# Performance work log

Measured on AMD Instinct MI355X. Metric: run time of the kernel, lower is better.

The kernel has to match this reference:

```python
import jax, jax.numpy as jnp
import numpy as np

B, C, H, W = 16, 256, 64, 64
NH, WS = 8, 8  # num_heads, window_size
HD = C // NH   # head_dim = 32


def setup_inputs() -> dict:
    key = jax.random.key(0)
    k1, k2, k3 = jax.random.split(key, 3)
    x = jax.random.normal(k1, (B, C, H, W), dtype=jnp.float32)
    w_qkv = jax.random.normal(k2, (3 * C, C), dtype=jnp.float32) * 0.02  # 1x1 conv, no bias
    w_proj = jax.random.normal(k3, (C, C), dtype=jnp.float32) * 0.02
    return {"x": x, "w_qkv": w_qkv, "w_proj": w_proj, "shift": 1}


def _window_partition(t, ws):
    # [b,c,h,w] -> [b*(h/ws)*(w/ws), ws*ws, c]
    b, c, h, w = t.shape
    t = t.reshape(b, c, h // ws, ws, w // ws, ws)
    t = t.transpose(0, 2, 4, 3, 5, 1)
    return t.reshape(-1, ws * ws, c)


def _window_reverse(t, b, c, h, w, ws):
    t = t.reshape(b, h // ws, w // ws, ws, ws, c)
    t = t.transpose(0, 5, 1, 3, 2, 4)
    return t.reshape(b, c, h, w)


def reference(x, w_qkv, w_proj, shift):
    b, c, h, w = x.shape
    ws = min(WS, h, w)
    shift_size = ws // 2 if (shift and ws > 1 and h % ws == 0 and w % ws == 0) else 0
    if shift_size > 0:
        x = jnp.roll(x, (-shift_size, -shift_size), axis=(2, 3))
    # 1x1 conv QKV: [b,c,h,w] x [3c,c] -> [b,3c,h,w]
    qkv = jnp.einsum('bchw,oc->bohw', x, w_qkv)
    q, k, v = jnp.split(qkv, 3, axis=1)
    q_t = _window_partition(q, ws)  # [Bw, S, c], S = ws*ws
    k_t = _window_partition(k, ws)
    v_t = _window_partition(v, ws)
    bw, s, _ = q_t.shape
    # heads: [Bw, nh, S, hd]
    qh = q_t.reshape(bw, s, NH, HD).transpose(0, 2, 1, 3)
    kh = k_t.reshape(bw, s, NH, HD).transpose(0, 2, 1, 3)
    vh = v_t.reshape(bw, s, NH, HD).transpose(0, 2, 1, 3)
    scale = 1.0 / jnp.sqrt(jnp.asarray(HD, dtype=qh.dtype))
    scores = jnp.einsum('bnqd,bnkd->bnqk', qh, kh) * scale
    attn = jax.nn.softmax(scores, axis=-1)
    out = jnp.einsum('bnqk,bnkd->bnqd', attn, vh)
    out = out.transpose(0, 2, 1, 3).reshape(bw, s, c)
    out = _window_reverse(out, b, c, h, w, ws)
    if shift_size > 0:
        out = jnp.roll(out, (shift_size, shift_size), axis=(2, 3))
    return jnp.einsum('bchw,oc->bohw', out, w_proj)
```

## Files before the change

### kernel.cpp

```cpp
#include <hip/hip_runtime.h>

typedef short bf16x8 __attribute__((ext_vector_type(8)));
typedef float f32x4 __attribute__((ext_vector_type(4)));
typedef unsigned short u16;
typedef unsigned int u32;

static __device__ __forceinline__ u16 f2bf(float f) {
  u32 u = __builtin_bit_cast(u32, f);
  u32 r = (u + 0x7FFFu + ((u >> 16) & 1u)) >> 16;
  return (u16)r;
}

__global__ __launch_bounds__(256) void k_conv(
    const float* __restrict__ wqkv, const float* __restrict__ wproj,
    u16* __restrict__ wbf) {
  const int cid = blockIdx.x * 256 + threadIdx.x;
  const float* src;
  int dst;
  if (cid < 24576) {
    const int tile = cid >> 9, rem = cid & 511;
    const int k = rem >> 6, lane = rem & 63;
    src = wqkv + (size_t)(tile * 16 + (lane & 15)) * 256 + k * 32 + (lane >> 4) * 8;
    dst = cid;
  } else {
    const int pid = cid - 24576;
    const int mt = pid >> 9, rem = pid & 511;
    const int h = rem >> 6, lane = rem & 63;
    src = wproj + (size_t)(mt * 16 + (lane & 15)) * 256 + h * 32 + (lane >> 4) * 8;
    dst = 24576 + h * 1024 + mt * 64 + lane;
  }
  float4 f0 = *(const float4*)(src);
  float4 f1 = *(const float4*)(src + 4);
  ushort4 a, b;
  a.x = f2bf(f0.x); a.y = f2bf(f0.y); a.z = f2bf(f0.z); a.w = f2bf(f0.w);
  b.x = f2bf(f1.x); b.y = f2bf(f1.y); b.z = f2bf(f1.z); b.w = f2bf(f1.w);
  *(ushort4*)(wbf + (size_t)dst * 8) = a;
  *(ushort4*)(wbf + (size_t)dst * 8 + 4) = b;
}

#define BUF0 0
#define BUF1 4096
#define XB 0
#define QH 8192
#define KH 10752
#define VTH 13312
#define PH 15616
#define LDS_TOT 20224

#define MEMF() asm volatile("" ::: "memory")
#define BAR()                        \
  do {                               \
    MEMF();                          \
    __builtin_amdgcn_s_barrier();    \
    MEMF();                          \
  } while (0)
#define WVM2() asm volatile("s_waitcnt vmcnt(2)" ::: "memory")
#define WVM0() asm volatile("s_waitcnt vmcnt(0)" ::: "memory")
#define WLG0() asm volatile("s_waitcnt lgkmcnt(0)" ::: "memory")

#define GL2LDS(gp, lp)                                   \
  __builtin_amdgcn_global_load_lds(                      \
      (__attribute__((address_space(1))) void*)(gp),     \
      (__attribute__((address_space(3))) void*)(lp), 16, 0, 0)

static __device__ __forceinline__ void stage_half(const u16* g, u16* l, int t) {
#pragma unroll
  for (int j = 0; j < 2; ++j) {
    const int off = (j * 256 + t) * 8;
    GL2LDS(g + off, l + off);
  }
}

#define QKV_TILE(BUFB, DSTB, U)                                           \
  do {                                                                    \
    const u16* wb_ = LDS + (BUFB) + lane * 8;                             \
    f32x4 acc = {0.f, 0.f, 0.f, 0.f};                                     \
    _Pragma("unroll") for (int k = 0; k < 8; ++k) acc =                   \
        __builtin_amdgcn_mfma_f32_16x16x32_bf16(                          \
            af[k], *(const bf16x8*)(wb_ + k * 512), acc, 0, 0, 0);        \
    _Pragma("unroll") for (int r = 0; r < 4; ++r)                         \
        LDS[(DSTB) + (pos0 + r) * 40 + (U) * 16 + l15] = f2bf(acc[r]);    \
  } while (0)

#define V_TILE(BUFB, U)                                                   \
  do {                                                                    \
    const u16* wb_ = LDS + (BUFB) + lane * 8;                             \
    f32x4 acc = {0.f, 0.f, 0.f, 0.f};                                     \
    _Pragma("unroll") for (int k = 0; k < 8; ++k) acc =                   \
        __builtin_amdgcn_mfma_f32_16x16x32_bf16(                          \
            af[k], *(const bf16x8*)(wb_ + k * 512), acc, 0, 0, 0);        \
    ushort4 pk;                                                           \
    pk.x = f2bf(acc[0]); pk.y = f2bf(acc[1]);                             \
    pk.z = f2bf(acc[2]); pk.w = f2bf(acc[3]);                             \
    *(ushort4*)&LDS[VTH + ((U) * 16 + l15) * 72 + pos0] = pk;             \
  } while (0)

__global__ __launch_bounds__(256, 4) void k_fused(
    const float* __restrict__ x, const u16* __restrict__ wbf,
    const int* __restrict__ shiftp, float* __restrict__ out) {
  __shared__ u16 LDS[LDS_TOT];
  const int blk = blockIdx.x;
  const int win = ((blk & 127) << 3) | (blk >> 7);
  const int b = win >> 6, wh = (win >> 3) & 7, ww = win & 7;
  const int off = (shiftp[0] != 0) ? 4 : 0;
  const int t = threadIdx.x;

  {
    u16* X = LDS + XB;
    const int wr = t & 7;
    const int h = ((wh << 3) + wr + off) & 63;
    const int w0 = ((ww << 3) + off) & 63;
    const int w1 = ((ww << 3) + off + 4) & 63;
    const int p0 = wr << 3;
#pragma unroll
    for (int it = 0; it < 8; ++it) {
      const int c = (t >> 3) + (it << 5);
      const float* src = x + ((size_t)(b * 256 + c) * 64 + h) * 64;
      float4 v0 = *(const float4*)(src + w0);
      float4 v1 = *(const float4*)(src + w1);
      X[(p0 + 0) * 264 + c] = f2bf(v0.x);
      X[(p0 + 1) * 264 + c] = f2bf(v0.y);
      X[(p0 + 2) * 264 + c] = f2bf(v0.z);
      X[(p0 + 3) * 264 + c] = f2bf(v0.w);
      X[(p0 + 4) * 264 + c] = f2bf(v1.x);
      X[(p0 + 5) * 264 + c] = f2bf(v1.y);
      X[(p0 + 6) * 264 + c] = f2bf(v1.z);
      X[(p0 + 7) * 264 + c] = f2bf(v1.w);
    }
  }
  __syncthreads();

  const int lane = t & 63, wv = t >> 6;
  const int l15 = lane & 15, quad = lane >> 4;
  const int pos0 = wv * 16 + quad * 4;

  bf16x8 af[8];
#pragma unroll
  for (int k = 0; k < 8; ++k)
    af[k] = *(const bf16x8*)&LDS[XB + (wv * 16 + l15) * 264 + quad * 8 + k * 32];
  WLG0();
  BAR();

  stage_half(wbf, LDS + BUF0, t);
  stage_half(wbf + 4096, LDS + BUF1, t);

  f32x4 accP[16];
#pragma unroll
  for (int mt = 0; mt < 16; ++mt) accP[mt] = (f32x4){0.f, 0.f, 0.f, 0.f};

  const float scale = 0.17677669529663687f;
  u16* Pw = LDS + PH + wv * 1152;

#pragma unroll 1
  for (int h = 0; h < 8; ++h) {
    WVM2(); BAR();
    QKV_TILE(BUF0, QH, 0);
    WLG0(); BAR();
    stage_half(wbf + (size_t)(16 + h * 2) * 4096, LDS + BUF0, t);
    WVM2(); BAR();
    QKV_TILE(BUF1, QH, 1);
    WLG0(); BAR();
    stage_half(wbf + (size_t)(17 + h * 2) * 4096, LDS + BUF1, t);
    WVM2(); BAR();
    QKV_TILE(BUF0, KH, 0);
    WLG0(); BAR();
    stage_half(wbf + (size_t)(32 + h * 2) * 4096, LDS + BUF0, t);
    WVM2(); BAR();
    QKV_TILE(BUF1, KH, 1);
    WLG0(); BAR();
    stage_half(wbf + (size_t)(33 + h * 2) * 4096, LDS + BUF1, t);
    WVM2(); BAR();
    V_TILE(BUF0, 0);
    WLG0(); BAR();
    stage_half(wbf + 196608 + (size_t)h * 8192, LDS + BUF0, t);
    WVM2(); BAR();
    V_TILE(BUF1, 1);
    WLG0(); BAR();
    stage_half(wbf + 196608 + (size_t)h * 8192 + 4096, LDS + BUF1, t);
    WVM2(); BAR();
    {
      bf16x8 aq = *(const bf16x8*)&LDS[QH + (wv * 16 + l15) * 40 + quad * 8];
      f32x4 sc[4];
#pragma unroll
      for (int nt = 0; nt < 4; ++nt) {
        bf16x8 bk = *(const bf16x8*)&LDS[KH + (nt * 16 + l15) * 40 + quad * 8];
        f32x4 z = {0.f, 0.f, 0.f, 0.f};
        sc[nt] = __builtin_amdgcn_mfma_f32_16x16x32_bf16(aq, bk, z, 0, 0, 0);
      }
#pragma unroll
      for (int r = 0; r < 4; ++r) {
        float mx = -1e30f;
#pragma unroll
        for (int nt = 0; nt < 4; ++nt) mx = fmaxf(mx, sc[nt][r]);
        mx = fmaxf(mx, __shfl_xor(mx, 1));
        mx = fmaxf(mx, __shfl_xor(mx, 2));
        mx = fmaxf(mx, __shfl_xor(mx, 4));
        mx = fmaxf(mx, __shfl_xor(mx, 8));
        float p[4], sum = 0.f;
#pragma unroll
        for (int nt = 0; nt < 4; ++nt) {
          p[nt] = __expf((sc[nt][r] - mx) * scale);
          sum += p[nt];
        }
        sum += __shfl_xor(sum, 1);
        sum += __shfl_xor(sum, 2);
        sum += __shfl_xor(sum, 4);
        sum += __shfl_xor(sum, 8);
        const float is = 1.f / sum;
#pragma unroll
        for (int nt = 0; nt < 4; ++nt)
          Pw[(quad * 4 + r) * 72 + nt * 16 + l15] = f2bf(p[nt] * is);
      }
      f32x4 oa[2];
      oa[0] = (f32x4){0.f, 0.f, 0.f, 0.f};
      oa[1] = (f32x4){0.f, 0.f, 0.f, 0.f};
#pragma unroll
      for (int kk = 0; kk < 2; ++kk) {
        bf16x8 ap = *(const bf16x8*)&Pw[l15 * 72 + kk * 32 + quad * 8];
#pragma unroll
        for (int n2 = 0; n2 < 2; ++n2) {
          bf16x8 bv =
              *(const bf16x8*)&LDS[VTH + (n2 * 16 + l15) * 72 + kk * 32 + quad * 8];
          oa[n2] = __builtin_amdgcn_mfma_f32_16x16x32_bf16(ap, bv, oa[n2], 0, 0, 0);
        }
      }
#pragma unroll
      for (int n2 = 0; n2 < 2; ++n2)
#pragma unroll
        for (int r = 0; r < 4; ++r)
          LDS[QH + (pos0 + r) * 40 + n2 * 16 + l15] = f2bf(oa[n2][r]);
      bf16x8 bo = *(const bf16x8*)&LDS[QH + (wv * 16 + l15) * 40 + quad * 8];
#pragma unroll
      for (int mt = 0; mt < 8; ++mt) {
        bf16x8 aw = *(const bf16x8*)&LDS[BUF0 + mt * 512 + lane * 8];
        accP[mt] = __builtin_amdgcn_mfma_f32_16x16x32_bf16(aw, bo, accP[mt], 0, 0, 0);
      }
      WLG0(); BAR();
      if (h < 7)
        stage_half(wbf + (size_t)((h + 1) * 2) * 4096, LDS + BUF0, t);
      if (h < 7) { WVM2(); } else { WVM0(); }
      BAR();
#pragma unroll
      for (int mt = 0; mt < 8; ++mt) {
        bf16x8 aw = *(const bf16x8*)&LDS[BUF1 + mt * 512 + lane * 8];
        accP[8 + mt] =
            __builtin_amdgcn_mfma_f32_16x16x32_bf16(aw, bo, accP[8 + mt], 0, 0, 0);
      }
    }
    WLG0(); BAR();
    if (h < 7)
      stage_half(wbf + (size_t)((h + 1) * 2 + 1) * 4096, LDS + BUF1, t);
  }

  const int pos = wv * 16 + l15;
  const int hco = ((wh << 3) + (pos >> 3) + off) & 63;
  const int wco = ((ww << 3) + (pos & 7) + off) & 63;
#pragma unroll
  for (int mt = 0; mt < 16; ++mt)
#pragma unroll
    for (int r = 0; r < 4; ++r) {
      const int c = mt * 16 + quad * 4 + r;
      out[((size_t)(b * 256 + c) << 12) + (hco << 6) + wco] = accP[mt][r];
    }
}

extern "C" void kernel_launch(void* const* d_in, const int* in_sizes, int n_in,
                              void* d_out, int out_size, void* d_ws, size_t ws_size,
                              hipStream_t stream) {
  const float* x = (const float*)d_in[0];
  const float* wqkv = (const float*)d_in[1];
  const float* wproj = (const float*)d_in[2];
  const int* shiftp = (const int*)d_in[3];
  float* outp = (float*)d_out;
  u16* wbf = (u16*)d_ws;
  hipLaunchKernelGGL(k_conv, dim3(128), dim3(256), 0, stream, wqkv, wproj, wbf);
  hipLaunchKernelGGL(k_fused, dim3(1024), dim3(256), 0, stream, x, wbf, shiftp, outp);
}
```

Baseline: 225.3 us.

## Merge double barriers into single wait-barrier-prefetch stage and stagger block starts

Each pair of barriers around a weight tile is replaced by one combined point that waits for all memory ops, then barriers, then issues the next tile's global-to-LDS load before computing on the current buffer. The second projection matmul moves after the loop-tail barrier so it overlaps the next prefetch. Blocks are also staggered with s_sleep based on their block index, to spread out contention on the weight reads. This halves the barrier count but keeps only one tile load in flight instead of two, so load latency may be exposed more often.

```diff
diff --git a/kernel.cpp b/kernel.cpp
--- a/kernel.cpp
+++ b/kernel.cpp
@@ -48,15 +48,12 @@
 #define LDS_TOT 20224
 
 #define MEMF() asm volatile("" ::: "memory")
-#define BAR()                        \
-  do {                               \
-    MEMF();                          \
-    __builtin_amdgcn_s_barrier();    \
-    MEMF();                          \
+#define ENTRY()                                                      \
+  do {                                                               \
+    asm volatile("s_waitcnt vmcnt(0) lgkmcnt(0)" ::: "memory");      \
+    __builtin_amdgcn_s_barrier();                                    \
+    MEMF();                                                          \
   } while (0)
-#define WVM2() asm volatile("s_waitcnt vmcnt(2)" ::: "memory")
-#define WVM0() asm volatile("s_waitcnt vmcnt(0)" ::: "memory")
-#define WLG0() asm volatile("s_waitcnt lgkmcnt(0)" ::: "memory")
 
 #define GL2LDS(gp, lp)                                   \
   __builtin_amdgcn_global_load_lds(                      \
@@ -104,6 +101,13 @@
   const int b = win >> 6, wh = (win >> 3) & 7, ww = win & 7;
   const int off = (shiftp[0] != 0) ? 4 : 0;
   const int t = threadIdx.x;
+
+  {
+    const int slot = (blk >> 8) & 3;
+    if (slot == 1) __builtin_amdgcn_s_sleep(16);
+    else if (slot == 2) __builtin_amdgcn_s_sleep(32);
+    else if (slot == 3) __builtin_amdgcn_s_sleep(48);
+  }
 
   {
     u16* X = LDS + XB;
@@ -138,11 +142,11 @@
 #pragma unroll
   for (int k = 0; k < 8; ++k)
     af[k] = *(const bf16x8*)&LDS[XB + (wv * 16 + l15) * 264 + quad * 8 + k * 32];
-  WLG0();
-  BAR();
+  asm volatile("s_waitcnt lgkmcnt(0)" ::: "memory");
+  __builtin_amdgcn_s_barrier();
+  MEMF();
 
   stage_half(wbf, LDS + BUF0, t);
-  stage_half(wbf + 4096, LDS + BUF1, t);
 
   f32x4 accP[16];
 #pragma unroll
@@ -150,34 +154,30 @@
 
   const float scale = 0.17677669529663687f;
   u16* Pw = LDS + PH + wv * 1152;
+  bf16x8 bo;
 
 #pragma unroll 1
   for (int h = 0; h < 8; ++h) {
-    WVM2(); BAR();
+    ENTRY();
+    stage_half(wbf + (size_t)(h * 2 + 1) * 4096, LDS + BUF1, t);
     QKV_TILE(BUF0, QH, 0);
-    WLG0(); BAR();
+    ENTRY();
     stage_half(wbf + (size_t)(16 + h * 2) * 4096, LDS + BUF0, t);
-    WVM2(); BAR();
     QKV_TILE(BUF1, QH, 1);
-    WLG0(); BAR();
+    ENTRY();
     stage_half(wbf + (size_t)(17 + h * 2) * 4096, LDS + BUF1, t);
-    WVM2(); BAR();
     QKV_TILE(BUF0, KH, 0);
-    WLG0(); BAR();
+    ENTRY();
     stage_half(wbf + (size_t)(32 + h * 2) * 4096, LDS + BUF0, t);
-    WVM2(); BAR();
     QKV_TILE(BUF1, KH, 1);
-    WLG0(); BAR();
+    ENTRY();
     stage_half(wbf + (size_t)(33 + h * 2) * 4096, LDS + BUF1, t);
-    WVM2(); BAR();
     V_TILE(BUF0, 0);
-    WLG0(); BAR();
+    ENTRY();
     stage_half(wbf + 196608 + (size_t)h * 8192, LDS + BUF0, t);
-    WVM2(); BAR();
     V_TILE(BUF1, 1);
-    WLG0(); BAR();
+    ENTRY();
     stage_half(wbf + 196608 + (size_t)h * 8192 + 4096, LDS + BUF1, t);
-    WVM2(); BAR();
     {
       bf16x8 aq = *(const bf16x8*)&LDS[QH + (wv * 16 + l15) * 40 + quad * 8];
       f32x4 sc[4];
@@ -229,27 +229,22 @@
 #pragma unroll
         for (int r = 0; r < 4; ++r)
           LDS[QH + (pos0 + r) * 40 + n2 * 16 + l15] = f2bf(oa[n2][r]);
-      bf16x8 bo = *(const bf16x8*)&LDS[QH + (wv * 16 + l15) * 40 + quad * 8];
+      bo = *(const bf16x8*)&LDS[QH + (wv * 16 + l15) * 40 + quad * 8];
 #pragma unroll
       for (int mt = 0; mt < 8; ++mt) {
         bf16x8 aw = *(const bf16x8*)&LDS[BUF0 + mt * 512 + lane * 8];
         accP[mt] = __builtin_amdgcn_mfma_f32_16x16x32_bf16(aw, bo, accP[mt], 0, 0, 0);
       }
-      WLG0(); BAR();
-      if (h < 7)
-        stage_half(wbf + (size_t)((h + 1) * 2) * 4096, LDS + BUF0, t);
-      if (h < 7) { WVM2(); } else { WVM0(); }
-      BAR();
-#pragma unroll
-      for (int mt = 0; mt < 8; ++mt) {
-        bf16x8 aw = *(const bf16x8*)&LDS[BUF1 + mt * 512 + lane * 8];
-        accP[8 + mt] =
-            __builtin_amdgcn_mfma_f32_16x16x32_bf16(aw, bo, accP[8 + mt], 0, 0, 0);
-      }
-    }
-    WLG0(); BAR();
+    }
+    ENTRY();
     if (h < 7)
-      stage_half(wbf + (size_t)((h + 1) * 2 + 1) * 4096, LDS + BUF1, t);
+      stage_half(wbf + (size_t)((h + 1) * 2) * 4096, LDS + BUF0, t);
+#pragma unroll
+    for (int mt = 0; mt < 8; ++mt) {
+      bf16x8 aw = *(const bf16x8*)&LDS[BUF1 + mt * 512 + lane * 8];
+      accP[8 + mt] =
+          __builtin_amdgcn_mfma_f32_16x16x32_bf16(aw, bo, accP[8 + mt], 0, 0, 0);
+    }
   }
 
   const int pos = wv * 16 + l15;
```

After: 222.4 us. Within noise of the previous version (-1.3%).
